# Kernel tuning notes

Measured on AMD Instinct MI355X. Metric: run time of the kernel, lower is better.

The kernel has to match this reference:

```python
import jax, jax.numpy as jnp
import numpy as np
import math

B, L, D = 2, 2048, 768
H, DK = 8, 64
DV = D // H  # 96
N_POS = 32
DFF = 2 * D
EPS = 1e-5


def setup_inputs() -> dict:
    key = jax.random.key(0)
    ks = jax.random.split(key, 12)
    s = 0.02
    return {
        "x": jax.random.normal(ks[0], (B, L, D), jnp.float32),
        "norm1_w": jnp.ones((D,), jnp.float32),
        "norm2_w": jnp.ones((D,), jnp.float32),
        "wq": jax.random.normal(ks[1], (D, H * DK), jnp.float32) * s,
        "wk": jax.random.normal(ks[2], (D, H * DK), jnp.float32) * s,
        "wv": jax.random.normal(ks[3], (D, H * DV), jnp.float32) * s,
        "wo": jax.random.normal(ks[4], (H * DV, D), jnp.float32) * s,
        "bo": jnp.zeros((D,), jnp.float32),
        "u_param": jax.random.normal(ks[5], (H, DK), jnp.float32) * s,
        "v_param": jax.random.normal(ks[6], (H, DK), jnp.float32) * s,
        "w_pos": jax.random.normal(ks[7], (H, DK, N_POS), jnp.float32) * s,
        "w1": jax.random.normal(ks[8], (D, DFF), jnp.float32) * s,
        "b1": jnp.zeros((DFF,), jnp.float32),
        "w2": jax.random.normal(ks[9], (DFF, D), jnp.float32) * s,
        "b2": jnp.zeros((D,), jnp.float32),
    }


def _rel_basis(l: int, n: int) -> jnp.ndarray:
    # Enformer-style central-mask relative position basis: [l, l, n]
    pos = jnp.arange(l)
    distance = pos[None, :] - pos[:, None]  # [l, l]
    pow_rate = jnp.exp(jnp.log(jnp.float32((l + 1) / 2.0)) / (n // 2))
    center_widths = pow_rate ** jnp.arange(1, n // 2 + 1, dtype=jnp.float32)
    d = distance[:, :, None].astype(jnp.float32)
    unsigned = (jnp.abs(d) <= center_widths).astype(jnp.float32)
    signed = jnp.sign(d) * unsigned
    return jnp.concatenate([unsigned, signed], axis=-1)  # [l, l, n]


def _rmsnorm(x, w):
    norm = jnp.mean(x * x, axis=-1, keepdims=True)
    return x * jax.lax.rsqrt(norm + EPS) * w


def reference(x, norm1_w, norm2_w, wq, wk, wv, wo, bo,
              u_param, v_param, w_pos, w1, b1, w2, b2):
    b, l, _ = x.shape
    skip = x
    h1 = _rmsnorm(x, norm1_w)

    q = (h1 @ wq).reshape(b, l, H, DK)
    k = (h1 @ wk).reshape(b, l, H, DK)
    v = (h1 @ wv).reshape(b, l, H, DV)

    basis = _rel_basis(l, N_POS)  # [l, l, n]
    scale = 1.0 / math.sqrt(DK)

    # qr_term: contract q with w_pos first, then with basis (avoids [h,l,l,d] r)
    qw = jnp.einsum('bihd,hdn->bihn', q, w_pos)          # [b,l,h,n]
    qr = jnp.einsum('bihn,ijn->bhij', qw, basis)          # [b,h,l,l]
    uk = jnp.einsum('hd,bjhd->bhj', u_param, k)[:, :, None, :]  # [b,h,1,l]
    vw = jnp.einsum('hd,hdn->hn', v_param, w_pos)         # [h,n]
    vr = jnp.einsum('hn,ijn->hij', vw, basis)[None]       # [1,h,l,l]

    bias = (qr + uk + vr) * scale
    scores = jnp.einsum('bihd,bjhd->bhij', q, k) * scale + bias
    attn = jax.nn.softmax(scores, axis=-1)
    out = jnp.einsum('bhij,bjhd->bihd', attn, v)          # [b,l,h,dv]

    out = out.reshape(b, l, H * DV) @ wo + bo
    x = out + skip

    skip = x
    h2 = _rmsnorm(x, norm2_w)
    h2 = jax.nn.gelu(h2 @ w1 + b1, approximate=False) @ w2 + b2
    return h2 + skip
```

## Files before the change

kernel.cpp:

```cpp
#include <hip/hip_runtime.h>

#define B_ 2
#define L_ 2048
#define D_ 768
#define H_ 8
#define DK_ 64
#define DV_ 96
#define NPOS_ 32

typedef __attribute__((ext_vector_type(8))) __bf16 bf16x8;
typedef __attribute__((ext_vector_type(4))) __bf16 bf16x4;
typedef __attribute__((ext_vector_type(4))) float f32x4;

static __device__ __forceinline__ float bs2f(short s) {
    return (float)__builtin_bit_cast(__bf16, s);
}
static __device__ __forceinline__ short f2bs(float f) {
    return __builtin_bit_cast(short, (__bf16)f);
}

__global__ __launch_bounds__(256) void prep_kernel(
    const float* __restrict__ wq, const float* __restrict__ wk,
    const float* __restrict__ wv, const float* __restrict__ wo,
    const float* __restrict__ w1, const float* __restrict__ w2,
    const float* __restrict__ vparam, const float* __restrict__ uparam,
    const float* __restrict__ wpos,
    short* __restrict__ wqkvT, short* __restrict__ woT,
    short* __restrict__ w1T, short* __restrict__ w2T,
    unsigned char* __restrict__ sidx, float* __restrict__ VU, float* __restrict__ VS,
    const float* __restrict__ x, const float* __restrict__ n1w, short* __restrict__ h1)
{
    __shared__ short T[64][66];
    __shared__ float vw[H_ * NPOS_];
    __shared__ float uw[H_ * NPOS_];
    __shared__ float red[4];
    int blk = blockIdx.x, tid = threadIdx.x;
    if (blk < 1056) {
        const float* W; short* Wt; int K, N, bx, by;
        if (blk < 96)       { W = wq; Wt = wqkvT;              K = 768;  N = 512;  int b = blk;       bx = b % 8;  by = b / 8; }
        else if (blk < 192) { W = wk; Wt = wqkvT + 512 * 768;  K = 768;  N = 512;  int b = blk - 96;  bx = b % 8;  by = b / 8; }
        else if (blk < 336) { W = wv; Wt = wqkvT + 1024 * 768; K = 768;  N = 768;  int b = blk - 192; bx = b % 12; by = b / 12; }
        else if (blk < 480) { W = wo; Wt = woT;                K = 768;  N = 768;  int b = blk - 336; bx = b % 12; by = b / 12; }
        else if (blk < 768) { W = w1; Wt = w1T;                K = 768;  N = 1536; int b = blk - 480; bx = b % 24; by = b / 24; }
        else                { W = w2; Wt = w2T;                K = 1536; N = 768;  int b = blk - 768; bx = b % 12; by = b / 12; }
        int n0 = bx << 6, k0 = by << 6;
        for (int idx = tid; idx < 4096; idx += 256) {
            int r = idx >> 6, c = idx & 63;
            T[c][r] = f2bs(W[(size_t)(k0 + r) * N + n0 + c]);
        }
        __syncthreads();
        for (int idx = tid; idx < 4096; idx += 256) {
            int r = idx >> 6, c = idx & 63;
            Wt[(size_t)(n0 + r) * K + k0 + c] = T[r][c];
        }
    } else if (blk == 1056) {
        float pr = expf(logf((L_ + 1) / 2.0f) / (NPOS_ / 2));
        for (int idx = tid; idx < 4095; idx += 256) {
            int d = idx - 2047;
            int ad = d < 0 ? -d : d;
            int c = 0;
            for (int m = 1; m <= NPOS_ / 2; ++m) {
                float cw = powf(pr, (float)m);
                if (cw < (float)ad) c++;
            }
            sidx[idx] = (unsigned char)(d > 0 ? c : (d < 0 ? 17 + c : 34));
        }
        {
            int h = tid >> 5, n = tid & 31;
            float av = 0.f, au = 0.f;
            for (int d = 0; d < DK_; ++d) {
                float wp = wpos[(h * DK_ + d) * NPOS_ + n];
                av += vparam[h * DK_ + d] * wp;
                au += uparam[h * DK_ + d] * wp;
            }
            vw[tid] = av;
            uw[tid] = au;
        }
        __syncthreads();
        if (tid < H_ * 17) {
            int h = tid / 17, m = tid % 17;
            float su = 0.f, ss = 0.f;
            for (int t2 = m; t2 < 16; ++t2) {
                su += vw[h * NPOS_ + t2] - uw[h * NPOS_ + t2];
                ss += vw[h * NPOS_ + 16 + t2] - uw[h * NPOS_ + 16 + t2];
            }
            VU[h * 17 + m] = su * 0.125f;
            VS[h * 17 + m] = ss * 0.125f;
        }
    } else {
        int row = blk - 1057;
        const float* xr = x + (size_t)row * D_;
        float ss = 0.f;
        for (int c = tid; c < D_; c += 256) { float f = xr[c]; ss += f * f; }
        for (int msk = 1; msk < 64; msk <<= 1) ss += __shfl_xor(ss, msk);
        if ((tid & 63) == 0) red[tid >> 6] = ss;
        __syncthreads();
        float tot = red[0] + red[1] + red[2] + red[3];
        float sc = rsqrtf(tot * (1.f / D_) + 1e-5f);
        for (int c = tid; c < D_; c += 256)
            h1[(size_t)row * D_ + c] = f2bs(xr[c] * sc * n1w[c]);
    }
}

__global__ __launch_bounds__(256) void rmsnorm_kernel(
    const float* __restrict__ x, const float* __restrict__ wgt, short* __restrict__ out)
{
    int row = blockIdx.x, tid = threadIdx.x;
    __shared__ float red[4];
    const float* xr = x + (size_t)row * D_;
    float ss = 0.f;
    for (int c = tid; c < D_; c += 256) { float f = xr[c]; ss += f * f; }
    for (int msk = 1; msk < 64; msk <<= 1) ss += __shfl_xor(ss, msk);
    if ((tid & 63) == 0) red[tid >> 6] = ss;
    __syncthreads();
    float tot = red[0] + red[1] + red[2] + red[3];
    float sc = rsqrtf(tot * (1.f / D_) + 1e-5f);
    for (int c = tid; c < D_; c += 256)
        out[(size_t)row * D_ + c] = f2bs(xr[c] * sc * wgt[c]);
}

__global__ __launch_bounds__(256) void gemm64(
    const short* __restrict__ A, const short* __restrict__ Bt,
    const float* __restrict__ bias, const float* __restrict__ resid,
    void* __restrict__ outp,
    int M, int N, int K, int act, int out_f32)
{
    __shared__ __align__(16) short Al[64 * 136];
    __shared__ __align__(16) short Bl[64 * 136];
    int tid = threadIdx.x;
    int w = tid >> 6, lane = tid & 63, quad = lane >> 4, t = lane & 15;
    int m0b = blockIdx.y << 6, n0b = blockIdx.x << 6;
    int wr = (w >> 1) << 5, wc = (w & 1) << 5;
    int rA = tid >> 4, c8 = (tid & 15) << 3;
    f32x4 acc[2][2] = {};
    bf16x8 pA[4], pB[4];
#pragma unroll
    for (int it = 0; it < 4; ++it) {
        pA[it] = *(const bf16x8*)&A[(size_t)(m0b + rA + (it << 4)) * K + c8];
        pB[it] = *(const bf16x8*)&Bt[(size_t)(n0b + rA + (it << 4)) * K + c8];
    }
    for (int kb = 0; kb < K; kb += 128) {
        __syncthreads();
#pragma unroll
        for (int it = 0; it < 4; ++it) {
            *(bf16x8*)&Al[(rA + (it << 4)) * 136 + c8] = pA[it];
            *(bf16x8*)&Bl[(rA + (it << 4)) * 136 + c8] = pB[it];
        }
        if (kb + 128 < K) {
#pragma unroll
            for (int it = 0; it < 4; ++it) {
                pA[it] = *(const bf16x8*)&A[(size_t)(m0b + rA + (it << 4)) * K + kb + 128 + c8];
                pB[it] = *(const bf16x8*)&Bt[(size_t)(n0b + rA + (it << 4)) * K + kb + 128 + c8];
            }
        }
        __syncthreads();
#pragma unroll
        for (int ks = 0; ks < 4; ++ks) {
            bf16x8 af0 = *(bf16x8*)&Al[(wr + t) * 136 + (ks << 5) + (quad << 3)];
            bf16x8 af1 = *(bf16x8*)&Al[(wr + 16 + t) * 136 + (ks << 5) + (quad << 3)];
            bf16x8 bf0 = *(bf16x8*)&Bl[(wc + t) * 136 + (ks << 5) + (quad << 3)];
            bf16x8 bf1 = *(bf16x8*)&Bl[(wc + 16 + t) * 136 + (ks << 5) + (quad << 3)];
            acc[0][0] = __builtin_amdgcn_mfma_f32_16x16x32_bf16(af0, bf0, acc[0][0], 0, 0, 0);
            acc[0][1] = __builtin_amdgcn_mfma_f32_16x16x32_bf16(af0, bf1, acc[0][1], 0, 0, 0);
            acc[1][0] = __builtin_amdgcn_mfma_f32_16x16x32_bf16(af1, bf0, acc[1][0], 0, 0, 0);
            acc[1][1] = __builtin_amdgcn_mfma_f32_16x16x32_bf16(af1, bf1, acc[1][1], 0, 0, 0);
        }
    }
#pragma unroll
    for (int ms = 0; ms < 2; ++ms)
#pragma unroll
        for (int ns = 0; ns < 2; ++ns)
#pragma unroll
            for (int r = 0; r < 4; ++r) {
                int row = m0b + wr + (ms << 4) + (quad << 2) + r;
                int col = n0b + wc + (ns << 4) + t;
                float v2 = acc[ms][ns][r];
                if (bias) v2 += bias[col];
                if (act == 1) v2 = 0.5f * v2 * (1.f + erff(v2 * 0.70710678118654752f));
                if (resid) v2 += resid[(size_t)row * N + col];
                if (out_f32) ((float*)outp)[(size_t)row * N + col] = v2;
                else ((short*)outp)[(size_t)row * N + col] = f2bs(v2);
            }
}

__global__ __launch_bounds__(256) void gemm128(
    const short* __restrict__ A, const short* __restrict__ Bt,
    const float* __restrict__ bias, const float* __restrict__ uadd,
    void* __restrict__ outp, int M, int N, int K, int act)
{
    __shared__ __align__(16) short Al[128 * 72];
    __shared__ __align__(16) short Bl[128 * 72];
    int tid = threadIdx.x;
    int w = tid >> 6, lane = tid & 63, quad = lane >> 4, t = lane & 15;
    int m0b = blockIdx.y << 7, n0b = blockIdx.x << 7;
    int wm = (w >> 1) << 6, wn = (w & 1) << 6;
    int r0 = tid >> 3, c8 = (tid & 7) << 3;
    f32x4 acc[4][4] = {};
    bf16x8 pA[4], pB[4];
#pragma unroll
    for (int it = 0; it < 4; ++it) {
        pA[it] = *(const bf16x8*)&A[(size_t)(m0b + r0 + (it << 5)) * K + c8];
        pB[it] = *(const bf16x8*)&Bt[(size_t)(n0b + r0 + (it << 5)) * K + c8];
    }
    for (int kb = 0; kb < K; kb += 64) {
        __syncthreads();
#pragma unroll
        for (int it = 0; it < 4; ++it) {
            *(bf16x8*)&Al[(r0 + (it << 5)) * 72 + c8] = pA[it];
            *(bf16x8*)&Bl[(r0 + (it << 5)) * 72 + c8] = pB[it];
        }
        if (kb + 64 < K) {
#pragma unroll
            for (int it = 0; it < 4; ++it) {
                pA[it] = *(const bf16x8*)&A[(size_t)(m0b + r0 + (it << 5)) * K + kb + 64 + c8];
                pB[it] = *(const bf16x8*)&Bt[(size_t)(n0b + r0 + (it << 5)) * K + kb + 64 + c8];
            }
        }
        __syncthreads();
#pragma unroll
        for (int ks = 0; ks < 2; ++ks) {
            bf16x8 af[4], bf[4];
#pragma unroll
            for (int ms = 0; ms < 4; ++ms)
                af[ms] = *(bf16x8*)&Al[(wm + ms * 16 + t) * 72 + (ks << 5) + (quad << 3)];
#pragma unroll
            for (int ns = 0; ns < 4; ++ns)
                bf[ns] = *(bf16x8*)&Bl[(wn + ns * 16 + t) * 72 + (ks << 5) + (quad << 3)];
#pragma unroll
            for (int ms = 0; ms < 4; ++ms)
#pragma unroll
                for (int ns = 0; ns < 4; ++ns)
                    acc[ms][ns] = __builtin_amdgcn_mfma_f32_16x16x32_bf16(af[ms], bf[ns], acc[ms][ns], 0, 0, 0);
        }
    }
#pragma unroll
    for (int ms = 0; ms < 4; ++ms)
#pragma unroll
        for (int ns = 0; ns < 4; ++ns)
#pragma unroll
            for (int r = 0; r < 4; ++r) {
                int row = m0b + wm + ms * 16 + (quad << 2) + r;
                int col = n0b + wn + ns * 16 + t;
                float v2 = acc[ms][ns][r];
                if (uadd && col < 512) v2 = 0.125f * (v2 + uadd[col]);
                if (bias) v2 += bias[col];
                if (act == 1) v2 = 0.5f * v2 * (1.f + erff(v2 * 0.70710678118654752f));
                ((short*)outp)[(size_t)row * N + col] = f2bs(v2);
            }
}

__global__ __launch_bounds__(256) void qv_kernel(
    const short* __restrict__ qkv, const float* __restrict__ wpos,
    const float* __restrict__ VU, const float* __restrict__ VS,
    float* __restrict__ Tg, short* __restrict__ vT)
{
    __shared__ __align__(16) char arena[69696];
    int blk = blockIdx.x, tid = threadIdx.x;
    if (blk < 256) {
        float* wl   = (float*)arena;
        float* qrow = (float*)(arena + 65536);
        float* qw   = (float*)(arena + 67584);
        float* sU   = (float*)(arena + 68608);
        float* sS   = (float*)(arena + 69152);
        for (int idx = tid; idx < 4096; idx += 256)
            ((float4*)wl)[idx] = ((const float4*)wpos)[idx];
        int r0 = blk << 4;
        int h = tid >> 5, n = tid & 31;
        for (int rr = 0; rr < 16; ++rr) {
            int row = r0 + rr;
            __syncthreads();
            const short* base = qkv + (size_t)row * 1792;
            qrow[tid]       = bs2f(base[tid]);
            qrow[tid + 256] = bs2f(base[tid + 256]);
            __syncthreads();
            float acc = 0.f;
            for (int d = 0; d < DK_; ++d)
                acc += qrow[h * DK_ + d] * wl[(h * DK_ + d) * 32 + n];
            qw[tid] = acc;
            __syncthreads();
            if (tid < 136) {
                int hh = tid / 17, m = tid % 17;
                float su = 0.f, ss = 0.f;
                for (int t2 = m; t2 < 16; ++t2) { su += qw[hh * NPOS_ + t2]; ss += qw[hh * NPOS_ + 16 + t2]; }
                sU[tid] = su + VU[tid];
                sS[tid] = ss + VS[tid];
            }
            __syncthreads();
            if (tid < 280) {
                int h2 = tid / 35, s = tid % 35;
                int m = s < 17 ? s : (s < 34 ? s - 17 : 0);
                float su = sU[h2 * 17 + m], ss = sS[h2 * 17 + m];
                Tg[(size_t)row * 280 + tid] = s < 17 ? su + ss : (s < 34 ? su - ss : su);
            }
        }
    } else {
        short* T = (short*)arena;
        int vb = blk - 256;
        int bh = vb >> 4, b = bh >> 3, h = bh & 7;
        int j0 = (vb & 15) << 7;
#pragma unroll
        for (int it = 0; it < 6; ++it) {
            int idx = tid + (it << 8);
            int row = idx / 12, c8 = (idx % 12) << 3;
            *(bf16x8*)&T[row * 104 + c8] =
                *(const bf16x8*)&qkv[(size_t)(b * L_ + j0 + row) * 1792 + 1024 + h * DV_ + c8];
        }
        __syncthreads();
#pragma unroll
        for (int it = 0; it < 6; ++it) {
            int idx = tid + (it << 8);
            int dv = idx >> 4;
            int q16 = idx & 15;
            int sub = q16 >> 3, k8 = q16 & 7;
            bf16x8 o;
#pragma unroll
            for (int c = 0; c < 8; ++c) {
                int jl = (sub << 6) + ((c & 3) << 4) + (k8 << 1) + (c >> 2);
                o[c] = __builtin_bit_cast(__bf16, T[jl * 104 + dv]);
            }
            *(bf16x8*)&vT[((size_t)bh * DV_ + dv) * L_ + j0 + (sub << 6) + (k8 << 3)] = o;
        }
    }
}

__global__ __launch_bounds__(512, 4) void flash_kernel(
    const short* __restrict__ qkv, const short* __restrict__ vT,
    const float* __restrict__ Tg, const unsigned char* __restrict__ sidx_g,
    short* __restrict__ ao)
{
    __shared__ __align__(16) char arena[77824];
    int tid = threadIdx.x;
    int w = tid >> 6, lane = tid & 63, quad = lane >> 4, t = lane & 15;
    int g = w >> 2, wg = w & 3, tg = tid & 255;
    short* Kl = (short*)(arena + g * 32256);
    short* Vt = (short*)(arena + g * 32256 + 9216);
    short* Pl = (short*)(arena + g * 32256 + 23040);
    float* Tt = (float*)(arena + 64512);
    unsigned char* sidxl = (unsigned char*)(arena + 73728);
    int bh = blockIdx.y, b = bh >> 3, h = bh & 7;
    int i0 = blockIdx.x << 6;

    for (int idx = tid; idx < 64 * 35; idx += 512) {
        int il = idx / 35, s = idx % 35;
        Tt[il * 36 + s] = Tg[(size_t)(b * L_ + i0 + il) * 280 + h * 35 + s];
    }
    for (int idx = tid; idx < 4095; idx += 512) sidxl[idx] = sidx_g[idx];

    int iq = i0 + wg * 16 + t;
    const short* qbase = qkv + (size_t)(b * L_ + iq) * 1792 + h * DK_;
    bf16x8 qf0 = *(const bf16x8*)(qbase + (quad << 3));
    bf16x8 qf1 = *(const bf16x8*)(qbase + 32 + (quad << 3));

    f32x4 O[6] = {};
    float lsum[4] = {0.f, 0.f, 0.f, 0.f};

    int kr = tg >> 3, kc = (tg & 7) << 3;
    bf16x8 kpre[2], vpre[3];
    {
        int j0 = g << 6;
        const short* kb0 = &qkv[(size_t)(b * L_ + j0 + kr) * 1792 + 512 + h * DK_ + kc];
        kpre[0] = *(const bf16x8*)kb0;
        kpre[1] = *(const bf16x8*)(kb0 + (size_t)32 * 1792);
#pragma unroll
        for (int it = 0; it < 3; ++it) {
            int idx = tg + (it << 8);
            int row = idx >> 3, c8 = (idx & 7) << 3;
            vpre[it] = *(const bf16x8*)&vT[((size_t)bh * DV_ + row) * L_ + j0 + c8];
        }
    }

    for (int tix = 0; tix < 16; ++tix) {
        int j0 = ((tix << 1) + g) << 6;
        __syncthreads();
        *(bf16x8*)&Kl[kr * 72 + kc] = kpre[0];
        *(bf16x8*)&Kl[(kr + 32) * 72 + kc] = kpre[1];
#pragma unroll
        for (int it = 0; it < 3; ++it) {
            int idx = tg + (it << 8);
            int row = idx >> 3, c8 = (idx & 7) << 3;
            *(bf16x8*)&Vt[row * 72 + c8] = vpre[it];
        }
        {
            int jn = (tix < 15) ? ((((tix + 1) << 1) + g) << 6) : (g << 6);
            const short* kb0 = &qkv[(size_t)(b * L_ + jn + kr) * 1792 + 512 + h * DK_ + kc];
            kpre[0] = *(const bf16x8*)kb0;
            kpre[1] = *(const bf16x8*)(kb0 + (size_t)32 * 1792);
#pragma unroll
            for (int it = 0; it < 3; ++it) {
                int idx = tg + (it << 8);
                int row = idx >> 3, c8 = (idx & 7) << 3;
                vpre[it] = *(const bf16x8*)&vT[((size_t)bh * DV_ + row) * L_ + jn + c8];
            }
        }
        __syncthreads();

        f32x4 S[4];
#pragma unroll
        for (int ct = 0; ct < 4; ++ct) {
            bf16x8 b0 = *(bf16x8*)&Kl[(ct * 16 + t) * 72 + (quad << 3)];
            bf16x8 b1 = *(bf16x8*)&Kl[(ct * 16 + t) * 72 + 32 + (quad << 3)];
            f32x4 z = {};
            z = __builtin_amdgcn_mfma_f32_16x16x32_bf16(qf0, b0, z, 0, 0, 0);
            S[ct] = __builtin_amdgcn_mfma_f32_16x16x32_bf16(qf1, b1, z, 0, 0, 0);
        }
#pragma unroll
        for (int r = 0; r < 4; ++r) {
            int il = wg * 16 + (quad << 2) + r;
            int i = i0 + il;
            const float* Trow = &Tt[il * 36];
            bf16x4 pv;
#pragma unroll
            for (int ct = 0; ct < 4; ++ct) {
                int j = j0 + ct * 16 + t;
                int s = sidxl[j - i + 2047];
                float p = __expf(S[ct][r] + Trow[s]);
                __bf16 pb = (__bf16)p;
                pv[ct] = pb;
                lsum[r] += (float)pb;
            }
            *(bf16x4*)&Pl[il * 72 + t * 4] = pv;
        }
#pragma unroll
        for (int ks = 0; ks < 2; ++ks) {
            bf16x8 pa = *(bf16x8*)&Pl[(wg * 16 + t) * 72 + (ks << 5) + (quad << 3)];
#pragma unroll
            for (int dv = 0; dv < 6; ++dv) {
                bf16x8 vb = *(bf16x8*)&Vt[(dv * 16 + t) * 72 + (ks << 5) + (quad << 3)];
                O[dv] = __builtin_amdgcn_mfma_f32_16x16x32_bf16(pa, vb, O[dv], 0, 0, 0);
            }
        }
    }

    __syncthreads();
    float* F = (float*)arena;
    int l2 = (wg << 6) + lane;
    if (g == 1) {
#pragma unroll
        for (int dv = 0; dv < 6; ++dv)
#pragma unroll
            for (int r = 0; r < 4; ++r)
                F[((dv << 2) + r) * 256 + l2] = O[dv][r];
#pragma unroll
        for (int r = 0; r < 4; ++r) F[(24 + r) * 256 + l2] = lsum[r];
    }
    __syncthreads();
    if (g == 0) {
#pragma unroll
        for (int r = 0; r < 4; ++r) {
            float lr = lsum[r] + F[(24 + r) * 256 + l2];
            lr += __shfl_xor(lr, 1);
            lr += __shfl_xor(lr, 2);
            lr += __shfl_xor(lr, 4);
            lr += __shfl_xor(lr, 8);
            float inv = 1.f / lr;
            int i = i0 + wg * 16 + (quad << 2) + r;
            size_t base = (size_t)(b * L_ + i) * D_ + h * DV_;
#pragma unroll
            for (int dv = 0; dv < 6; ++dv)
                ao[base + dv * 16 + t] = f2bs((O[dv][r] + F[((dv << 2) + r) * 256 + l2]) * inv);
        }
    }
}

extern "C" void kernel_launch(void* const* d_in, const int* in_sizes, int n_in,
                              void* d_out, int out_size, void* d_ws, size_t ws_size,
                              hipStream_t stream)
{
    const float* x    = (const float*)d_in[0];
    const float* n1w  = (const float*)d_in[1];
    const float* n2w  = (const float*)d_in[2];
    const float* wq   = (const float*)d_in[3];
    const float* wk   = (const float*)d_in[4];
    const float* wv   = (const float*)d_in[5];
    const float* wo   = (const float*)d_in[6];
    const float* bo   = (const float*)d_in[7];
    const float* up   = (const float*)d_in[8];
    const float* vp   = (const float*)d_in[9];
    const float* wpos = (const float*)d_in[10];
    const float* w1   = (const float*)d_in[11];
    const float* b1   = (const float*)d_in[12];
    const float* w2   = (const float*)d_in[13];
    const float* b2   = (const float*)d_in[14];

    char* ws = (char*)d_ws;
    short* h1   = (short*)(ws + 0);
    short* qkv  = (short*)(ws + 6291456);
    float* Tg   = (float*)(ws + 20971520);
    float* VUg  = (float*)(ws + 25559040);
    float* VSg  = (float*)(ws + 25560064);
    unsigned char* sidx = (unsigned char*)(ws + 25561088);
    short* ao   = (short*)(ws + 25569280);
    float* x2   = (float*)(ws + 31860736);
    short* vT   = (short*)(ws + 31860736);
    short* wqkvT= (short*)(ws + 44443648);
    short* woT  = (short*)(ws + 47196160);
    short* w1T  = (short*)(ws + 48375808);
    short* w2T  = (short*)(ws + 50735104);
    short* f1   = (short*)(ws + 0);
    short* h2n  = (short*)(ws + 14680064);

    prep_kernel<<<5153, 256, 0, stream>>>(wq, wk, wv, wo, w1, w2, vp, up, wpos,
                                          wqkvT, woT, w1T, w2T, sidx, VUg, VSg,
                                          x, n1w, h1);
    gemm128<<<dim3(14, 32), 256, 0, stream>>>(h1, wqkvT, nullptr, up, qkv, 4096, 1792, 768, 0);
    qv_kernel<<<512, 256, 0, stream>>>(qkv, wpos, VUg, VSg, Tg, vT);
    flash_kernel<<<dim3(32, 16), 512, 0, stream>>>(qkv, vT, Tg, sidx, ao);
    gemm64<<<dim3(12, 64), 256, 0, stream>>>(ao, woT, bo, x, x2, 4096, 768, 768, 0, 1);
    rmsnorm_kernel<<<4096, 256, 0, stream>>>(x2, n2w, h2n);
    gemm128<<<dim3(12, 32), 256, 0, stream>>>(h2n, w1T, b1, nullptr, f1, 4096, 1536, 768, 1);
    gemm64<<<dim3(12, 64), 256, 0, stream>>>(f1, w2T, b2, x2, d_out, 4096, 768, 1536, 0, 1);
}
```

Baseline: 313.1 us.

## Pre-swizzle V into MFMA fragment layout and load directly to registers

```diff
diff --git a/kernel.cpp b/kernel.cpp
--- a/kernel.cpp
+++ b/kernel.cpp
@@ -309,16 +309,19 @@
 #pragma unroll
         for (int it = 0; it < 6; ++it) {
             int idx = tid + (it << 8);
-            int dv = idx >> 4;
-            int q16 = idx & 15;
-            int sub = q16 >> 3, k8 = q16 & 7;
+            int sub = idx / 768;
+            int rem = idx - sub * 768;
+            int f = rem >> 6, l = rem & 63;
+            int dv = f >> 1, ks = f & 1;
+            int q = l >> 4, t = l & 15;
             bf16x8 o;
 #pragma unroll
-            for (int c = 0; c < 8; ++c) {
-                int jl = (sub << 6) + ((c & 3) << 4) + (k8 << 1) + (c >> 2);
-                o[c] = __builtin_bit_cast(__bf16, T[jl * 104 + dv]);
-            }
-            *(bf16x8*)&vT[((size_t)bh * DV_ + dv) * L_ + j0 + (sub << 6) + (k8 << 3)] = o;
+            for (int e = 0; e < 8; ++e) {
+                int jl = ((e & 3) << 4) + (ks << 3) + (q << 1) + (e >> 2);
+                o[e] = __builtin_bit_cast(__bf16, T[(sub * 64 + jl) * 104 + dv * 16 + t]);
+            }
+            int jt = ((vb & 15) << 1) + sub;
+            *(bf16x8*)&vT[((((size_t)bh * 32 + jt) * 12 + f) * 64 + l) * 8] = o;
         }
     }
 }
@@ -328,15 +331,14 @@
     const float* __restrict__ Tg, const unsigned char* __restrict__ sidx_g,
     short* __restrict__ ao)
 {
-    __shared__ __align__(16) char arena[77824];
+    __shared__ __align__(16) char arena[50176];
     int tid = threadIdx.x;
     int w = tid >> 6, lane = tid & 63, quad = lane >> 4, t = lane & 15;
     int g = w >> 2, wg = w & 3, tg = tid & 255;
-    short* Kl = (short*)(arena + g * 32256);
-    short* Vt = (short*)(arena + g * 32256 + 9216);
-    short* Pl = (short*)(arena + g * 32256 + 23040);
-    float* Tt = (float*)(arena + 64512);
-    unsigned char* sidxl = (unsigned char*)(arena + 73728);
+    short* Kl = (short*)(arena + g * 18432);
+    short* Pl = (short*)(arena + g * 18432 + 9216);
+    float* Tt = (float*)(arena + 36864);
+    unsigned char* sidxl = (unsigned char*)(arena + 46080);
     int bh = blockIdx.y, b = bh >> 3, h = bh & 7;
     int i0 = blockIdx.x << 6;
 
@@ -355,46 +357,35 @@
     float lsum[4] = {0.f, 0.f, 0.f, 0.f};
 
     int kr = tg >> 3, kc = (tg & 7) << 3;
-    bf16x8 kpre[2], vpre[3];
+    bf16x8 kpre[2];
     {
         int j0 = g << 6;
         const short* kb0 = &qkv[(size_t)(b * L_ + j0 + kr) * 1792 + 512 + h * DK_ + kc];
         kpre[0] = *(const bf16x8*)kb0;
         kpre[1] = *(const bf16x8*)(kb0 + (size_t)32 * 1792);
-#pragma unroll
-        for (int it = 0; it < 3; ++it) {
-            int idx = tg + (it << 8);
-            int row = idx >> 3, c8 = (idx & 7) << 3;
-            vpre[it] = *(const bf16x8*)&vT[((size_t)bh * DV_ + row) * L_ + j0 + c8];
-        }
-    }
+    }
+    const short* vfb = vT + (size_t)bh * 32 * 12 * 512 + lane * 8;
 
     for (int tix = 0; tix < 16; ++tix) {
         int j0 = ((tix << 1) + g) << 6;
+        int jt = j0 >> 6;
         __syncthreads();
         *(bf16x8*)&Kl[kr * 72 + kc] = kpre[0];
         *(bf16x8*)&Kl[(kr + 32) * 72 + kc] = kpre[1];
-#pragma unroll
-        for (int it = 0; it < 3; ++it) {
-            int idx = tg + (it << 8);
-            int row = idx >> 3, c8 = (idx & 7) << 3;
-            *(bf16x8*)&Vt[row * 72 + c8] = vpre[it];
-        }
+        bf16x8 vfrag[12];
+#pragma unroll
+        for (int f = 0; f < 12; ++f)
+            vfrag[f] = *(const bf16x8*)(vfb + ((size_t)jt * 12 + f) * 512);
         {
             int jn = (tix < 15) ? ((((tix + 1) << 1) + g) << 6) : (g << 6);
             const short* kb0 = &qkv[(size_t)(b * L_ + jn + kr) * 1792 + 512 + h * DK_ + kc];
             kpre[0] = *(const bf16x8*)kb0;
             kpre[1] = *(const bf16x8*)(kb0 + (size_t)32 * 1792);
-#pragma unroll
-            for (int it = 0; it < 3; ++it) {
-                int idx = tg + (it << 8);
-                int row = idx >> 3, c8 = (idx & 7) << 3;
-                vpre[it] = *(const bf16x8*)&vT[((size_t)bh * DV_ + row) * L_ + jn + c8];
-            }
         }
         __syncthreads();
 
         f32x4 S[4];
+        __builtin_amdgcn_s_setprio(1);
 #pragma unroll
         for (int ct = 0; ct < 4; ++ct) {
             bf16x8 b0 = *(bf16x8*)&Kl[(ct * 16 + t) * 72 + (quad << 3)];
@@ -403,6 +394,7 @@
             z = __builtin_amdgcn_mfma_f32_16x16x32_bf16(qf0, b0, z, 0, 0, 0);
             S[ct] = __builtin_amdgcn_mfma_f32_16x16x32_bf16(qf1, b1, z, 0, 0, 0);
         }
+        __builtin_amdgcn_s_setprio(0);
 #pragma unroll
         for (int r = 0; r < 4; ++r) {
             int il = wg * 16 + (quad << 2) + r;
@@ -420,15 +412,15 @@
             }
             *(bf16x4*)&Pl[il * 72 + t * 4] = pv;
         }
+        __builtin_amdgcn_s_setprio(1);
 #pragma unroll
         for (int ks = 0; ks < 2; ++ks) {
             bf16x8 pa = *(bf16x8*)&Pl[(wg * 16 + t) * 72 + (ks << 5) + (quad << 3)];
 #pragma unroll
-            for (int dv = 0; dv < 6; ++dv) {
-                bf16x8 vb = *(bf16x8*)&Vt[(dv * 16 + t) * 72 + (ks << 5) + (quad << 3)];
-                O[dv] = __builtin_amdgcn_mfma_f32_16x16x32_bf16(pa, vb, O[dv], 0, 0, 0);
-            }
-        }
+            for (int dv = 0; dv < 6; ++dv)
+                O[dv] = __builtin_amdgcn_mfma_f32_16x16x32_bf16(pa, vfrag[dv * 2 + ks], O[dv], 0, 0, 0);
+        }
+        __builtin_amdgcn_s_setprio(0);
     }
 
     __syncthreads();
```

Result: no change. 309.1 us (-1.3%).
